# Performance work log

Hardware: AMD Instinct MI355X
Metric: run time of the kernel (lower is better)

The kernel has to match this reference:

```python
import math
import jax, jax.numpy as jnp
import numpy as np

N_HEADS = 32
N_KV_HEADS = 8
HEAD_DIM = 64
DIM = 2048
SEQ = 4096
EST_Q = 64          # idx = min(64, seqlen)
VERTICAL_SIZE = 300 # min(prompt_len, max(300, 30))
SLASH_SIZE = 800    # min(prompt_len, max(800, 50))


def apply_rope(t, cos, sin):
    # t: [B,S,H,hd]; pairs are consecutive (reshape(...,-1,2) in torch view_as_complex)
    B, S, H, hd = t.shape
    tr = t.reshape(B, S, H, hd // 2, 2)
    xr, xi = tr[..., 0], tr[..., 1]
    c = cos[None, :, None, :]
    s = sin[None, :, None, :]
    orr = xr * c - xi * s
    oii = xr * s + xi * c
    return jnp.stack([orr, oii], axis=-1).reshape(B, S, H, hd)


def sum_all_diagonal(mat):
    # faithful jax version of torch as_strided trick: sum over anti-shifted diagonals
    # mat: [b,h,n,m] -> [b,h,n+m-1]; sum_diags[j] = sum_i mat[i, i + j - n], j in [1, n+m-1]
    b, h, n, m = mat.shape
    padded = jnp.pad(mat, ((0, 0), (0, 0), (0, 0), (n, n)))
    gidx = jnp.arange(n)[:, None] + jnp.arange(n + m)[None, :]  # [n, n+m]
    diags = jnp.take_along_axis(padded, jnp.broadcast_to(gidx, (b, h, n, n + m)), axis=-1)
    return diags.sum(axis=2)[:, :, 1:]


def setup_inputs() -> dict:
    key = jax.random.key(0)
    ks = jax.random.split(key, 6)
    x = jax.random.normal(ks[0], (1, SEQ, DIM), dtype=jnp.float32)
    # real RoPE tables (theta = 10000)
    inv_freq = 1.0 / (10000.0 ** (np.arange(0, HEAD_DIM, 2, dtype=np.float32) / HEAD_DIM))
    ang = np.outer(np.arange(SEQ, dtype=np.float32), inv_freq)  # [S, hd/2]
    freqs_cos = jnp.asarray(np.cos(ang), dtype=jnp.float32)
    freqs_sin = jnp.asarray(np.sin(ang), dtype=jnp.float32)
    scale = 0.02
    wq = jax.random.normal(ks[1], (DIM, N_HEADS * HEAD_DIM), dtype=jnp.float32) * scale
    wk = jax.random.normal(ks[2], (DIM, N_KV_HEADS * HEAD_DIM), dtype=jnp.float32) * scale
    wv = jax.random.normal(ks[3], (DIM, N_KV_HEADS * HEAD_DIM), dtype=jnp.float32) * scale
    wo = jax.random.normal(ks[4], (N_HEADS * HEAD_DIM, DIM), dtype=jnp.float32) * scale
    return {"x": x, "freqs_cos": freqs_cos, "freqs_sin": freqs_sin,
            "wq": wq, "wk": wk, "wv": wv, "wo": wo}


def reference(x, freqs_cos, freqs_sin, wq, wk, wv, wo):
    B, S, D = x.shape
    H, Hkv, hd = N_HEADS, N_KV_HEADS, HEAD_DIM
    rep = H // Hkv
    scale = 1.0 / math.sqrt(hd)

    # QKV + RoPE (K gets RoPE, V does not), GQA repeat
    q = apply_rope((x @ wq).reshape(B, S, H, hd), freqs_cos, freqs_sin).transpose(0, 2, 1, 3)
    k = apply_rope((x @ wk).reshape(B, S, Hkv, hd), freqs_cos, freqs_sin)
    v = (x @ wv).reshape(B, S, Hkv, hd)
    k = jnp.repeat(k, rep, axis=2).transpose(0, 2, 1, 3)  # [B,H,S,hd]
    v = jnp.repeat(v, rep, axis=2).transpose(0, 2, 1, 3)

    # --- vertical / slash pattern estimation (first idx queries, as in source) ---
    idx = min(EST_Q, S)
    qe = q[:, :, :idx, :]
    est = jnp.einsum('bhqd,bhkd->bhqk', qe, k) * scale  # [B,H,idx,S]
    ar = jnp.arange(idx)
    blk = ar[:, None] >= ar[None, :]
    tail = jnp.where(blk[None, None], est[..., -idx:], -jnp.inf)
    est = jnp.concatenate([est[..., :S - idx], tail], axis=-1)
    probs = jax.nn.softmax(est, axis=-1)

    Vn = min(S, VERTICAL_SIZE)
    Sl = min(S, SLASH_SIZE)
    vertical = probs.sum(axis=2)                  # [B,H,S]
    _, v_idx = jax.lax.top_k(vertical, Vn)        # [B,H,Vn]
    diag = sum_all_diagonal(probs)[..., :S]       # [..., :-idx+1] -> length S
    _, s_idx = jax.lax.top_k(diag, Sl)
    slash = S - 1 - s_idx                         # [B,H,Sl]

    sparse_keys = jnp.sort(jnp.concatenate([v_idx, slash], axis=-1), axis=-1)  # [B,H,K]

    # --- sparse causal attention over selected keys ---
    k_sp = jnp.take_along_axis(k, sparse_keys[..., None], axis=2)  # [B,H,K,hd]
    v_sp = jnp.take_along_axis(v, sparse_keys[..., None], axis=2)
    att = jnp.einsum('bhqd,bhkd->bhqk', q, k_sp) * scale           # [B,H,S,K]
    causal = sparse_keys[:, :, None, :] <= jnp.arange(S)[None, None, :, None]
    att = jnp.where(causal, att, -1e30)
    p = jax.nn.softmax(att, axis=-1)
    out = jnp.einsum('bhqk,bhkd->bhqd', p, v_sp)
    out = out.transpose(0, 2, 1, 3).reshape(B, S, H * hd)
    return out @ wo
```

## Files before the change

kernel.cpp:

```cpp
#include <hip/hip_runtime.h>
#include <hip/hip_bf16.h>
#include <math.h>
#include <stdint.h>

#define SEQ   4096
#define DIMM  2048
#define NH    32
#define NKV   8
#define HD    64
#define NSP   1100
#define NSPP  1152

typedef __bf16 bf16x8 __attribute__((ext_vector_type(8)));
typedef float  f32x4  __attribute__((ext_vector_type(4)));

__device__ inline void split8(const float* __restrict__ p, bf16x8& h, bf16x8& l) {
#pragma unroll
    for (int i = 0; i < 8; ++i) {
        float v = p[i];
        __bf16 hv = (__bf16)v;
        h[i] = hv;
        l[i] = (__bf16)(v - (float)hv);
    }
}
__device__ inline f32x4 load4(const void* __restrict__ p, size_t idx, bool f) {
    if (f) return *(const f32x4*)((const float*)p + idx);
    const __bf16* b = (const __bf16*)p + idx;
    f32x4 v;
    v[0] = (float)b[0]; v[1] = (float)b[1]; v[2] = (float)b[2]; v[3] = (float)b[3];
    return v;
}
__device__ __forceinline__ void gl_lds16(const __bf16* __restrict__ g, __bf16* l) {
    __builtin_amdgcn_global_load_lds(
        (const __attribute__((address_space(1))) void*)g,
        (__attribute__((address_space(3))) void*)l, 16, 0, 0);
}

__global__ __launch_bounds__(256) void detect_k(const void* __restrict__ x,
                                                int* __restrict__ flag) {
    const __bf16* p = (const __bf16*)x;
    int tid = threadIdx.x;
    bool bad = false;
    for (int i = 0; i < 16; ++i) {
        float v = fabsf((float)p[tid * 16 + i]);
        if (!(v <= 1e10f)) bad = true;
    }
    unsigned long long m = __ballot(bad);
    __shared__ unsigned long long w[4];
    if ((tid & 63) == 0) w[tid >> 6] = m;
    __syncthreads();
    if (tid == 0) flag[0] = ((w[0] | w[1] | w[2] | w[3]) != 0ULL) ? 1 : 0;
}

__global__ __launch_bounds__(256) void convert_x_k(const void* __restrict__ x,
                                                   __bf16* __restrict__ xb,
                                                   const int* __restrict__ flag) {
    int i0 = (blockIdx.x * 256 + threadIdx.x) * 8;
    if (*flag) {
        const float* xf = (const float*)x;
        bf16x8 o;
        for (int i = 0; i < 8; ++i) o[i] = (__bf16)xf[i0 + i];
        *(bf16x8*)(xb + i0) = o;
    } else {
        *(bf16x8*)(xb + i0) = *(const bf16x8*)((const __bf16*)x + i0);
    }
}

__global__ __launch_bounds__(256) void transpose_cvt_k(const void* __restrict__ in,
                                                       __bf16* __restrict__ out, int R, int C,
                                                       const int* __restrict__ flag) {
    __shared__ __bf16 tile[32][33];
    bool f = (*flag != 0);
    int cb = blockIdx.x * 32, rb = blockIdx.y * 32;
    int tx = threadIdx.x & 31, ty = threadIdx.x >> 5;
    for (int i = 0; i < 32; i += 8) {
        size_t idx = (size_t)(rb + ty + i) * C + cb + tx;
        float v = f ? ((const float*)in)[idx] : (float)((const __bf16*)in)[idx];
        tile[ty + i][tx] = (__bf16)v;
    }
    __syncthreads();
    for (int i = 0; i < 32; i += 8)
        out[(size_t)(cb + ty + i) * R + rb + tx] = tile[tx][ty + i];
}

__global__ __launch_bounds__(256) void gemm_nt_k(const __bf16* __restrict__ A,
                                                 const __bf16* __restrict__ Bt,
                                                 void* __restrict__ C, int M, int N, int K,
                                                 int f32out, const int* __restrict__ flag) {
    int bm = blockIdx.x, bn = blockIdx.y;
    __shared__ __bf16 As[128 * 64];
    __shared__ __bf16 Bs[128 * 64];
    int tid = threadIdx.x, wave = tid >> 6, lane = tid & 63;
    int quad = lane >> 4, l16 = lane & 15;
    int wm = (wave >> 1) * 64, wn = (wave & 1) * 64;
    const f32x4 z4 = {0.f, 0.f, 0.f, 0.f};
    f32x4 acc[4][4];
    for (int a = 0; a < 4; ++a) for (int b = 0; b < 4; ++b) acc[a][b] = z4;
    const __bf16* Ab = A  + (size_t)(bm * 128) * K;
    const __bf16* Bb = Bt + (size_t)(bn * 128) * K;
    for (int k0 = 0; k0 < K; k0 += 64) {
#pragma unroll
        for (int it = 0; it < 4; ++it) {
            int ci = it * 256 + tid;
            int row = ci >> 3, c8 = (ci & 7) * 8;
            gl_lds16(Ab + (size_t)row * K + k0 + c8, As + ci * 8);
            gl_lds16(Bb + (size_t)row * K + k0 + c8, Bs + ci * 8);
        }
        __syncthreads();
#pragma unroll
        for (int ks = 0; ks < 2; ++ks) {
            bf16x8 af[4], bfr[4];
#pragma unroll
            for (int mt = 0; mt < 4; ++mt)
                af[mt]  = *(const bf16x8*)&As[(wm + mt * 16 + l16) * 64 + ks * 32 + quad * 8];
#pragma unroll
            for (int nt = 0; nt < 4; ++nt)
                bfr[nt] = *(const bf16x8*)&Bs[(wn + nt * 16 + l16) * 64 + ks * 32 + quad * 8];
#pragma unroll
            for (int mt = 0; mt < 4; ++mt)
#pragma unroll
                for (int nt = 0; nt < 4; ++nt)
                    acc[mt][nt] = __builtin_amdgcn_mfma_f32_16x16x32_bf16(af[mt], bfr[nt], acc[mt][nt], 0, 0, 0);
        }
        __syncthreads();
    }
    bool f32o = f32out && (*flag != 0);
    for (int mt = 0; mt < 4; ++mt)
        for (int nt = 0; nt < 4; ++nt) {
            int rowb = bm * 128 + wm + mt * 16 + quad * 4;
            int col  = bn * 128 + wn + nt * 16 + l16;
            if (f32o) {
                for (int r = 0; r < 4; ++r)
                    ((float*)C)[(size_t)(rowb + r) * N + col] = acc[mt][nt][r];
            } else {
                for (int r = 0; r < 4; ++r)
                    ((__bf16*)C)[(size_t)(rowb + r) * N + col] = (__bf16)acc[mt][nt][r];
            }
        }
}

__device__ __forceinline__ void gemm_split_body(const void* __restrict__ A,
                                                const void* __restrict__ B,
                                                float* __restrict__ C,
                                                int N, int K, bool f, int bm, int bn,
                                                float Asf[][36], float Bsf[][36]) {
    int tid = threadIdx.x, wave = tid >> 6, lane = tid & 63;
    int quad = lane >> 4, l16 = lane & 15;
    int wm = (wave >> 1) * 64, wn = (wave & 1) * 64;
    const f32x4 z4 = {0.f, 0.f, 0.f, 0.f};
    f32x4 acc[4][4];
    for (int a = 0; a < 4; ++a) for (int b = 0; b < 4; ++b) acc[a][b] = z4;
    int arow = tid >> 1, acol = (tid & 1) * 16;
    for (int k0 = 0; k0 < K; k0 += 32) {
        for (int g = 0; g < 4; ++g) {
            f32x4 v = load4(A, (size_t)(bm * 128 + arow) * K + k0 + acol + g * 4, f);
            *(f32x4*)&Asf[arow][acol + g * 4] = v;
        }
        for (int it = 0; it < 4; ++it) {
            int g = tid + it * 256;
            int krow = g >> 5, ng = (g & 31) * 4;
            f32x4 v = load4(B, (size_t)(k0 + krow) * N + bn * 128 + ng, f);
            Bsf[ng + 0][krow] = v[0];
            Bsf[ng + 1][krow] = v[1];
            Bsf[ng + 2][krow] = v[2];
            Bsf[ng + 3][krow] = v[3];
        }
        __syncthreads();
        bf16x8 ah[4], al[4], bh[4], bl[4];
        for (int mt = 0; mt < 4; ++mt) split8(&Asf[wm + mt * 16 + l16][quad * 8], ah[mt], al[mt]);
        for (int nt = 0; nt < 4; ++nt) split8(&Bsf[wn + nt * 16 + l16][quad * 8], bh[nt], bl[nt]);
        for (int mt = 0; mt < 4; ++mt)
            for (int nt = 0; nt < 4; ++nt) {
                acc[mt][nt] = __builtin_amdgcn_mfma_f32_16x16x32_bf16(al[mt], bh[nt], acc[mt][nt], 0, 0, 0);
                acc[mt][nt] = __builtin_amdgcn_mfma_f32_16x16x32_bf16(ah[mt], bl[nt], acc[mt][nt], 0, 0, 0);
                acc[mt][nt] = __builtin_amdgcn_mfma_f32_16x16x32_bf16(ah[mt], bh[nt], acc[mt][nt], 0, 0, 0);
            }
        __syncthreads();
    }
    for (int mt = 0; mt < 4; ++mt)
        for (int nt = 0; nt < 4; ++nt)
            for (int r = 0; r < 4; ++r)
                C[(size_t)(bm * 128 + wm + mt * 16 + quad * 4 + r) * N + bn * 128 + wn + nt * 16 + l16] = acc[mt][nt][r];
}

__global__ __launch_bounds__(256) void gemm_split_dual_k(const void* __restrict__ x,
                                                         const void* __restrict__ wk,
                                                         float* __restrict__ Kf,
                                                         const void* __restrict__ wq,
                                                         float* __restrict__ Qe,
                                                         const int* __restrict__ flag) {
    __shared__ float Asf[128][36];
    __shared__ float Bsf[128][36];
    bool f = (*flag != 0);
    if (blockIdx.x < 32) {
        if (blockIdx.y >= 4) return;
        gemm_split_body(x, wk, Kf, 512, 2048, f, blockIdx.x, blockIdx.y, Asf, Bsf);
    } else {
        gemm_split_body(x, wq, Qe, 2048, 2048, f, 0, blockIdx.y, Asf, Bsf);
    }
}

__global__ __launch_bounds__(256) void rope_all_k(__bf16* __restrict__ Qb,
                                                  float* __restrict__ Kf,
                                                  float* __restrict__ Qe,
                                                  __bf16* __restrict__ Kb,
                                                  const void* __restrict__ fc,
                                                  const void* __restrict__ fs,
                                                  const int* __restrict__ flag) {
    int bx = blockIdx.x;
    bool fl = (*flag != 0);
    if (bx < 4096) {
        int idx = bx * 256 + threadIdx.x;
        int t = idx >> 8;
        int r = idx & 255;
        int hh = r >> 3;
        int j4 = r & 7;
        __bf16* p = Qb + (size_t)t * DIMM + hh * HD + j4 * 8;
        float c[4], s[4];
        if (fl) {
            f32x4 cv = *(const f32x4*)((const float*)fc + t * 32 + j4 * 4);
            f32x4 sv = *(const f32x4*)((const float*)fs + t * 32 + j4 * 4);
#pragma unroll
            for (int i = 0; i < 4; ++i) { c[i] = cv[i]; s[i] = sv[i]; }
        } else {
            const __bf16* cb = (const __bf16*)fc + t * 32 + j4 * 4;
            const __bf16* sb = (const __bf16*)fs + t * 32 + j4 * 4;
#pragma unroll
            for (int i = 0; i < 4; ++i) { c[i] = (float)cb[i]; s[i] = (float)sb[i]; }
        }
        bf16x8 v = *(const bf16x8*)p;
        bf16x8 o;
#pragma unroll
        for (int i = 0; i < 4; ++i) {
            float xr = (float)v[2 * i], xi = (float)v[2 * i + 1];
            o[2 * i]     = (__bf16)(xr * c[i] - xi * s[i]);
            o[2 * i + 1] = (__bf16)(xr * s[i] + xi * c[i]);
        }
        *(bf16x8*)p = o;
    } else {
        int idx = (bx - 4096) * 256 + threadIdx.x;
        const int NKP = SEQ * NKV * 32;
        const int NQP = 64 * NH * 32;
        float* p; int t, j;
        bool isK = (idx < NKP);
        size_t koff = 0;
        if (isK) {
            t = idx >> 8; int r = idx & 255; j = r & 31;
            koff = (size_t)t * (NKV * HD) + (r >> 5) * HD + 2 * j;
            p = Kf + koff;
        } else {
            int k = idx - NKP;
            if (k >= NQP) return;
            t = k >> 10; int r = k & 1023; j = r & 31;
            p = Qe + (size_t)t * DIMM + (r >> 5) * HD + 2 * j;
        }
        float c, s;
        if (fl) {
            c = ((const float*)fc)[t * 32 + j];
            s = ((const float*)fs)[t * 32 + j];
        } else {
            c = (float)((const __bf16*)fc)[t * 32 + j];
            s = (float)((const __bf16*)fs)[t * 32 + j];
        }
        float xr = p[0], xi = p[1];
        float o0 = xr * c - xi * s;
        float o1 = xr * s + xi * c;
        p[0] = o0;
        p[1] = o1;
        if (isK) {
            __bf16* kb = Kb + koff;
            kb[0] = (__bf16)o0;
            kb[1] = (__bf16)o1;
        }
    }
}

__global__ __launch_bounds__(256) void est_part_k(const float* __restrict__ Qe,
                                                  const float* __restrict__ Kf,
                                                  float* __restrict__ pm,
                                                  float* __restrict__ ps,
                                                  float* __restrict__ diag) {
    int h = blockIdx.x, sl = blockIdx.y;
    int tid = threadIdx.x, wave = tid >> 6, lane = tid & 63;
    int quad = lane >> 4, l16 = lane & 15;
    for (int i = tid; i < 512; i += 256) diag[h * SEQ + sl * 512 + i] = 0.f;
    __shared__ float Ml[64];
    __shared__ float pA[4][64];
    bf16x8 qh[4][2], ql[4][2];
    for (int mt = 0; mt < 4; ++mt)
        for (int kc = 0; kc < 2; ++kc)
            split8(Qe + (size_t)(mt * 16 + l16) * DIMM + h * HD + kc * 32 + quad * 8,
                   qh[mt][kc], ql[mt][kc]);
    int kvoff = (h >> 2) * HD;
    float pmax[4][4];
    for (int mt = 0; mt < 4; ++mt) for (int r = 0; r < 4; ++r) pmax[mt][r] = -3.0e38f;
    for (int jb = wave; jb < 8; jb += 4)
        for (int c = 0; c < 4; ++c) {
            int j0 = sl * 512 + jb * 64 + c * 16;
            const float* kp = Kf + (size_t)(j0 + l16) * (NKV * HD) + kvoff + quad * 8;
            bf16x8 kh0, kl0, kh1, kl1;
            split8(kp, kh0, kl0);
            split8(kp + 32, kh1, kl1);
            int j = j0 + l16;
            for (int mt = 0; mt < 4; ++mt) {
                f32x4 acc = {0.f, 0.f, 0.f, 0.f};
                acc = __builtin_amdgcn_mfma_f32_16x16x32_bf16(ql[mt][0], kh0, acc, 0, 0, 0);
                acc = __builtin_amdgcn_mfma_f32_16x16x32_bf16(qh[mt][0], kl0, acc, 0, 0, 0);
                acc = __builtin_amdgcn_mfma_f32_16x16x32_bf16(qh[mt][0], kh0, acc, 0, 0, 0);
                acc = __builtin_amdgcn_mfma_f32_16x16x32_bf16(ql[mt][1], kh1, acc, 0, 0, 0);
                acc = __builtin_amdgcn_mfma_f32_16x16x32_bf16(qh[mt][1], kl1, acc, 0, 0, 0);
                acc = __builtin_amdgcn_mfma_f32_16x16x32_bf16(qh[mt][1], kh1, acc, 0, 0, 0);
                for (int r = 0; r < 4; ++r) {
                    int q = mt * 16 + quad * 4 + r;
                    float sv = acc[r] * 0.125f;
                    if (j >= SEQ - 64 && q < j - (SEQ - 64)) sv = -1e30f;
                    pmax[mt][r] = fmaxf(pmax[mt][r], sv);
                }
            }
        }
    for (int mt = 0; mt < 4; ++mt)
        for (int r = 0; r < 4; ++r)
            for (int m2 = 1; m2 < 16; m2 <<= 1)
                pmax[mt][r] = fmaxf(pmax[mt][r], __shfl_xor(pmax[mt][r], m2));
    if (l16 == 0)
        for (int mt = 0; mt < 4; ++mt)
            for (int r = 0; r < 4; ++r)
                pA[wave][mt * 16 + quad * 4 + r] = pmax[mt][r];
    __syncthreads();
    if (tid < 64)
        Ml[tid] = fmaxf(fmaxf(pA[0][tid], pA[1][tid]), fmaxf(pA[2][tid], pA[3][tid]));
    __syncthreads();
    float mreg[4][4];
    for (int mt = 0; mt < 4; ++mt)
        for (int r = 0; r < 4; ++r)
            mreg[mt][r] = Ml[mt * 16 + quad * 4 + r];
    float psum[4][4];
    for (int mt = 0; mt < 4; ++mt) for (int r = 0; r < 4; ++r) psum[mt][r] = 0.f;
    for (int jb = wave; jb < 8; jb += 4)
        for (int c = 0; c < 4; ++c) {
            int j0 = sl * 512 + jb * 64 + c * 16;
            const float* kp = Kf + (size_t)(j0 + l16) * (NKV * HD) + kvoff + quad * 8;
            bf16x8 kh0, kl0, kh1, kl1;
            split8(kp, kh0, kl0);
            split8(kp + 32, kh1, kl1);
            int j = j0 + l16;
            for (int mt = 0; mt < 4; ++mt) {
                f32x4 acc = {0.f, 0.f, 0.f, 0.f};
                acc = __builtin_amdgcn_mfma_f32_16x16x32_bf16(ql[mt][0], kh0, acc, 0, 0, 0);
                acc = __builtin_amdgcn_mfma_f32_16x16x32_bf16(qh[mt][0], kl0, acc, 0, 0, 0);
                acc = __builtin_amdgcn_mfma_f32_16x16x32_bf16(qh[mt][0], kh0, acc, 0, 0, 0);
                acc = __builtin_amdgcn_mfma_f32_16x16x32_bf16(ql[mt][1], kh1, acc, 0, 0, 0);
                acc = __builtin_amdgcn_mfma_f32_16x16x32_bf16(qh[mt][1], kl1, acc, 0, 0, 0);
                acc = __builtin_amdgcn_mfma_f32_16x16x32_bf16(qh[mt][1], kh1, acc, 0, 0, 0);
                for (int r = 0; r < 4; ++r) {
                    int q = mt * 16 + quad * 4 + r;
                    float sv = acc[r] * 0.125f;
                    if (j >= SEQ - 64 && q < j - (SEQ - 64)) sv = -1e30f;
                    psum[mt][r] += __expf(sv - mreg[mt][r]);
                }
            }
        }
    for (int mt = 0; mt < 4; ++mt)
        for (int r = 0; r < 4; ++r)
            for (int m2 = 1; m2 < 16; m2 <<= 1)
                psum[mt][r] += __shfl_xor(psum[mt][r], m2);
    if (l16 == 0)
        for (int mt = 0; mt < 4; ++mt)
            for (int r = 0; r < 4; ++r)
                pA[wave][mt * 16 + quad * 4 + r] = psum[mt][r];
    __syncthreads();
    if (tid < 64) {
        pm[(h * 8 + sl) * 64 + tid] = Ml[tid];
        ps[(h * 8 + sl) * 64 + tid] = pA[0][tid] + pA[1][tid] + pA[2][tid] + pA[3][tid];
    }
}

__global__ __launch_bounds__(256) void vert_diag_k(const float* __restrict__ Qe,
                                                   const float* __restrict__ Kf,
                                                   const float* __restrict__ pm,
                                                   const float* __restrict__ ps,
                                                   float* __restrict__ vert,
                                                   float* __restrict__ diag) {
    int h = blockIdx.x, jb = blockIdx.y;
    int tid = threadIdx.x, wave = tid >> 6, lane = tid & 63;
    int quad = lane >> 4, l16 = lane & 15;
    __shared__ float P[64][132];
    __shared__ float dloc[192];
    __shared__ float rm_l[64], rs_l[64];
    for (int i = tid; i < 192; i += 256) dloc[i] = 0.f;
    if (tid < 64) {
        float M = -3.0e38f;
        for (int sl = 0; sl < 8; ++sl) M = fmaxf(M, pm[(h * 8 + sl) * 64 + tid]);
        float S = 0.f;
        for (int sl = 0; sl < 8; ++sl)
            S += ps[(h * 8 + sl) * 64 + tid] * __expf(pm[(h * 8 + sl) * 64 + tid] - M);
        rm_l[tid] = M;
        rs_l[tid] = S;
    }
    bf16x8 qh[4][2], ql[4][2];
    for (int mt = 0; mt < 4; ++mt)
        for (int kc = 0; kc < 2; ++kc)
            split8(Qe + (size_t)(mt * 16 + l16) * DIMM + h * HD + kc * 32 + quad * 8,
                   qh[mt][kc], ql[mt][kc]);
    __syncthreads();
    float rm[4][4], rs[4][4];
    for (int mt = 0; mt < 4; ++mt)
        for (int r = 0; r < 4; ++r) {
            int q = mt * 16 + quad * 4 + r;
            rm[mt][r] = rm_l[q];
            rs[mt][r] = rs_l[q];
        }
    int kvoff = (h >> 2) * HD;
    for (int c = 0; c < 2; ++c) {
        int jl0 = wave * 32 + c * 16;
        int j0 = jb * 128 + jl0;
        const float* kp = Kf + (size_t)(j0 + l16) * (NKV * HD) + kvoff + quad * 8;
        bf16x8 kh0, kl0, kh1, kl1;
        split8(kp, kh0, kl0);
        split8(kp + 32, kh1, kl1);
        int j = j0 + l16;
        for (int mt = 0; mt < 4; ++mt) {
            f32x4 acc = {0.f, 0.f, 0.f, 0.f};
            acc = __builtin_amdgcn_mfma_f32_16x16x32_bf16(ql[mt][0], kh0, acc, 0, 0, 0);
            acc = __builtin_amdgcn_mfma_f32_16x16x32_bf16(qh[mt][0], kl0, acc, 0, 0, 0);
            acc = __builtin_amdgcn_mfma_f32_16x16x32_bf16(qh[mt][0], kh0, acc, 0, 0, 0);
            acc = __builtin_amdgcn_mfma_f32_16x16x32_bf16(ql[mt][1], kh1, acc, 0, 0, 0);
            acc = __builtin_amdgcn_mfma_f32_16x16x32_bf16(qh[mt][1], kl1, acc, 0, 0, 0);
            acc = __builtin_amdgcn_mfma_f32_16x16x32_bf16(qh[mt][1], kh1, acc, 0, 0, 0);
            for (int r = 0; r < 4; ++r) {
                int q = mt * 16 + quad * 4 + r;
                float sv = acc[r] * 0.125f;
                if (j >= SEQ - 64 && q < j - (SEQ - 64)) sv = -1e30f;
                P[q][jl0 + l16] = __expf(sv - rm[mt][r]) / rs[mt][r];
            }
        }
    }
    __syncthreads();
    if (tid < 128) {
        float vacc = 0.f;
        for (int q = 0; q < 64; ++q) {
            float pb = P[q][tid];
            vacc += pb;
            if (jb * 128 + tid + 63 - q < SEQ) atomicAdd(&dloc[tid + 63 - q], pb);
        }
        vert[h * SEQ + jb * 128 + tid] = vacc;
    }
    __syncthreads();
    for (int i = tid; i < 192; i += 256) {
        int g = jb * 128 + i;
        if (g < SEQ) atomicAdd(&diag[h * SEQ + g], dloc[i]);
    }
}

__global__ __launch_bounds__(256) void topk_merge_k(const float* __restrict__ vert,
                                                    const float* __restrict__ diag,
                                                    int* __restrict__ skeys) {
    __shared__ int cnt[4096];
    __shared__ int hist4[4][256];
    __shared__ int scanb[256];
    __shared__ int B_sh, kk_sh;
    int h = blockIdx.x, tid = threadIdx.x, wave = tid >> 6;
    for (int i = tid; i < 4096; i += 256) cnt[i] = 0;
    __syncthreads();
    for (int selp = 0; selp < 2; ++selp) {
        const float* vals = (selp == 0 ? vert : diag) + h * SEQ;
        int k = (selp == 0) ? 300 : 800;
        bool flip = (selp == 1);
        unsigned bits[16];
        for (int g = 0; g < 4; ++g) {
            f32x4 v = *(const f32x4*)(vals + tid * 16 + g * 4);
            for (int e = 0; e < 4; ++e) bits[g * 4 + e] = __float_as_uint(v[e]);
        }
        unsigned prefix = 0;
        int kk = k;
        for (int pass = 0; pass < 4; ++pass) {
            int sh = 8 * (3 - pass);
            for (int w = 0; w < 4; ++w) hist4[w][tid] = 0;
            __syncthreads();
            for (int e = 0; e < 16; ++e) {
                unsigned b = bits[e];
                bool in = (pass == 0) || ((b >> (sh + 8)) == prefix);
                if (in) atomicAdd(&hist4[wave][(b >> sh) & 255], 1);
            }
            __syncthreads();
            scanb[tid] = hist4[0][tid] + hist4[1][tid] + hist4[2][tid] + hist4[3][tid];
            __syncthreads();
            for (int off = 1; off < 256; off <<= 1) {
                int v = (tid + off < 256) ? scanb[tid + off] : 0;
                __syncthreads();
                scanb[tid] += v;
                __syncthreads();
            }
            int sufNext = (tid < 255) ? scanb[tid + 1] : 0;
            if (scanb[tid] >= kk && sufNext < kk) { B_sh = tid; kk_sh = kk - sufNext; }
            __syncthreads();
            prefix = (prefix << 8) | (unsigned)B_sh;
            kk = kk_sh;
            __syncthreads();
        }
        int localEq = 0;
        for (int e = 0; e < 16; ++e) {
            unsigned b = bits[e];
            if (b > prefix) {
                int idx = tid * 16 + e;
                atomicAdd(&cnt[flip ? (4095 - idx) : idx], 1);
            } else if (b == prefix) ++localEq;
        }
        scanb[tid] = localEq;
        __syncthreads();
        for (int off = 1; off < 256; off <<= 1) {
            int v = (tid >= off) ? scanb[tid - off] : 0;
            __syncthreads();
            scanb[tid] += v;
            __syncthreads();
        }
        int eqOff = scanb[tid] - localEq;
        int taken = 0;
        for (int e = 0; e < 16; ++e) {
            unsigned b = bits[e];
            if (b == prefix) {
                if (eqOff + taken < kk) {
                    int idx = tid * 16 + e;
                    atomicAdd(&cnt[flip ? (4095 - idx) : idx], 1);
                }
                ++taken;
            }
        }
        __syncthreads();
    }
    int base = tid * 16;
    int loc[16];
    int s = 0;
    for (int e = 0; e < 16; ++e) { loc[e] = s; s += cnt[base + e]; }
    scanb[tid] = s;
    __syncthreads();
    for (int off = 1; off < 256; off <<= 1) {
        int v = (tid >= off) ? scanb[tid - off] : 0;
        __syncthreads();
        scanb[tid] += v;
        __syncthreads();
    }
    int chunkExcl = scanb[tid] - s;
    int* out = skeys + h * NSPP;
    for (int e = 0; e < 16; ++e) {
        int c = cnt[base + e];
        int pos = chunkExcl + loc[e];
        for (int r = 0; r < c; ++r) out[pos + r] = base + e;
    }
    for (int i = NSP + tid; i < NSPP; i += 256) out[i] = 0x7fffffff;
}

__global__ __launch_bounds__(256) void gather_k(const __bf16* __restrict__ Kb,
                                                const __bf16* __restrict__ Vb,
                                                const int* __restrict__ skeys,
                                                __bf16* __restrict__ Ksp,
                                                __bf16* __restrict__ VspT) {
    int h = blockIdx.x, jb = blockIdx.y;
    __shared__ __bf16 tile[64][72];
    int tid = threadIdx.x;
    int jl = tid >> 2, d0 = (tid & 3) * 16;
    int j = jb * 64 + jl;
    int key = skeys[h * NSPP + j];
    int kv = (h >> 2) * HD;
    const bf16x8 z = {};
    bf16x8 k0v = z, k1v = z, v0v = z, v1v = z;
    if ((unsigned)key < SEQ) {
        const __bf16* ks = Kb + (size_t)key * (NKV * HD) + kv + d0;
        const __bf16* vs = Vb + (size_t)key * (NKV * HD) + kv + d0;
        k0v = *(const bf16x8*)ks; k1v = *(const bf16x8*)(ks + 8);
        v0v = *(const bf16x8*)vs; v1v = *(const bf16x8*)(vs + 8);
    }
    __bf16* kd = Ksp + ((size_t)h * NSPP + j) * HD + d0;
    *(bf16x8*)kd = k0v;
    *(bf16x8*)(kd + 8) = k1v;
    *(bf16x8*)&tile[jl][d0] = v0v;
    *(bf16x8*)&tile[jl][d0 + 8] = v1v;
    __syncthreads();
    int d = tid >> 2, jl0 = (tid & 3) * 16;
    bf16x8 o0, o1;
    for (int e = 0; e < 8; ++e) { o0[e] = tile[jl0 + e][d]; o1[e] = tile[jl0 + 8 + e][d]; }
    __bf16* vt = VspT + ((size_t)h * HD + d) * NSPP + jb * 64 + jl0;
    *(bf16x8*)vt = o0;
    *(bf16x8*)(vt + 8) = o1;
}

__global__ __launch_bounds__(512) void sparse_attn_k(const __bf16* __restrict__ Qb,
                                                     const __bf16* __restrict__ Ksp,
                                                     const __bf16* __restrict__ VspT,
                                                     const int* __restrict__ skeys,
                                                     __bf16* __restrict__ AO) {
    int qb = blockIdx.x, h = blockIdx.y;
    int tid = threadIdx.x, wave = tid >> 6, lane = tid & 63;
    int quad = lane >> 4, l16 = lane & 15;
    __shared__ __bf16 sc[64][1160];
    __shared__ float rsm[64];
    int t0 = qb * 64;
    bf16x8 aq[4][2];
#pragma unroll
    for (int qs = 0; qs < 4; ++qs)
#pragma unroll
        for (int kc = 0; kc < 2; ++kc)
            aq[qs][kc] = *(const bf16x8*)(Qb + (size_t)(t0 + qs * 16 + l16) * DIMM + h * HD + kc * 32 + quad * 8);
    const __bf16* Kh = Ksp + (size_t)h * NSPP * HD;
    const int* sk = skeys + h * NSPP;
#pragma unroll
    for (int c = 0; c < 9; ++c) {
        int j0 = wave * 144 + c * 16;
        const __bf16* kp = Kh + (size_t)(j0 + l16) * HD + quad * 8;
        bf16x8 b0 = *(const bf16x8*)kp;
        bf16x8 b1 = *(const bf16x8*)(kp + 32);
        int j = j0 + l16;
        int key = sk[j];
#pragma unroll
        for (int qs = 0; qs < 4; ++qs) {
            f32x4 acc = {0.f, 0.f, 0.f, 0.f};
            acc = __builtin_amdgcn_mfma_f32_16x16x32_bf16(aq[qs][0], b0, acc, 0, 0, 0);
            acc = __builtin_amdgcn_mfma_f32_16x16x32_bf16(aq[qs][1], b1, acc, 0, 0, 0);
            int qg = t0 + qs * 16 + quad * 4;
#pragma unroll
            for (int r = 0; r < 4; ++r) {
                float sv = acc[r] * 0.125f;
                if (key > qg + r) sv = -1e30f;
                sc[qs * 16 + quad * 4 + r][j] = (__bf16)sv;
            }
        }
    }
    __syncthreads();
    {
        int row = tid >> 3, sub = tid & 7;
        int c0 = sub * 144;
        float mx = -3.0e38f;
        for (int i = 0; i < 18; ++i) {
            bf16x8 v = *(const bf16x8*)&sc[row][c0 + i * 8];
            for (int e = 0; e < 8; ++e) mx = fmaxf(mx, (float)v[e]);
        }
        for (int m2 = 1; m2 < 8; m2 <<= 1) mx = fmaxf(mx, __shfl_xor(mx, m2, 8));
        float sm = 0.f;
        for (int i = 0; i < 18; ++i) {
            int cb = c0 + i * 8;
            bf16x8 v = *(const bf16x8*)&sc[row][cb];
            bf16x8 pw;
            for (int e = 0; e < 8; ++e) {
                float pv = 0.f;
                if (cb + e < NSP) { pv = __expf((float)v[e] - mx); sm += pv; }
                pw[e] = (__bf16)pv;
            }
            *(bf16x8*)&sc[row][cb] = pw;
        }
        for (int m2 = 1; m2 < 8; m2 <<= 1) sm += __shfl_xor(sm, m2, 8);
        if (sub == 0) rsm[row] = sm;
    }
    __syncthreads();
    int qs = wave >> 1, dh = wave & 1;
    const f32x4 z4 = {0.f, 0.f, 0.f, 0.f};
    f32x4 o0 = z4, o1 = z4;
    const __bf16* Vh = VspT + ((size_t)h * HD + dh * 32) * NSPP;
#pragma unroll 4
    for (int c = 0; c < 36; ++c) {
        int kb = c * 32;
        bf16x8 pa = *(const bf16x8*)&sc[qs * 16 + l16][kb + quad * 8];
        bf16x8 v0 = *(const bf16x8*)(Vh + (size_t)l16 * NSPP + kb + quad * 8);
        bf16x8 v1 = *(const bf16x8*)(Vh + (size_t)(16 + l16) * NSPP + kb + quad * 8);
        o0 = __builtin_amdgcn_mfma_f32_16x16x32_bf16(pa, v0, o0, 0, 0, 0);
        o1 = __builtin_amdgcn_mfma_f32_16x16x32_bf16(pa, v1, o1, 0, 0, 0);
    }
#pragma unroll
    for (int r = 0; r < 4; ++r) {
        int ql = qs * 16 + quad * 4 + r;
        float inv = 1.f / rsm[ql];
        size_t base = (size_t)(t0 + ql) * DIMM + h * HD + dh * 32;
        AO[base + l16]      = (__bf16)(o0[r] * inv);
        AO[base + 16 + l16] = (__bf16)(o1[r] * inv);
    }
}

extern "C" void kernel_launch(void* const* d_in, const int* in_sizes, int n_in,
                              void* d_out, int out_size, void* d_ws, size_t ws_size,
                              hipStream_t stream) {
    const void* x  = d_in[0];
    const void* fc = d_in[1];
    const void* fs = d_in[2];
    const void* wq = d_in[3];
    const void* wk = d_in[4];
    const void* wv = d_in[5];
    const void* wo = d_in[6];
    char* ws = (char*)d_ws;

    __bf16* Qb   = (__bf16*)(ws + 0);
    __bf16* Kb   = (__bf16*)(ws + 16777216);
    __bf16* Vb   = (__bf16*)(ws + 20971520);
    __bf16* xbf  = (__bf16*)(ws + 25165824);
    float*  Kf32 = (float*)(ws + 25165824);
    float*  Qef32= (float*)(ws + 33554432);
    __bf16* AO   = (__bf16*)(ws + 25165824);
    __bf16* Wt   = (__bf16*)(ws + 41943040);
    __bf16* Ksp  = (__bf16*)(ws + 41943040);
    __bf16* VspT = (__bf16*)(ws + 46661632);
    float*  vert = (float*)(ws + 51396608);
    float*  diag = (float*)(ws + 51920896);
    int*    skeys= (int*)(ws + 52445184);
    int*    flag = (int*)(ws + 52592640);
    float*  pm   = (float*)(ws + 52592896);
    float*  ps   = (float*)(ws + 52658432);

    dim3 b256(256);
    detect_k<<<1, b256, 0, stream>>>(x, flag);
    convert_x_k<<<4096, b256, 0, stream>>>(x, xbf, flag);
    transpose_cvt_k<<<dim3(64, 64), b256, 0, stream>>>(wq, Wt, 2048, 2048, flag);
    gemm_nt_k<<<dim3(32, 16), b256, 0, stream>>>(xbf, Wt, Qb, 4096, 2048, 2048, 0, flag);
    transpose_cvt_k<<<dim3(16, 64), b256, 0, stream>>>(wv, Wt, 2048, 512, flag);
    gemm_nt_k<<<dim3(32, 4), b256, 0, stream>>>(xbf, Wt, Vb, 4096, 512, 2048, 0, flag);
    gemm_split_dual_k<<<dim3(33, 16), b256, 0, stream>>>(x, wk, Kf32, wq, Qef32, flag);
    rope_all_k<<<8448, b256, 0, stream>>>(Qb, Kf32, Qef32, Kb, fc, fs, flag);
    est_part_k<<<dim3(32, 8), b256, 0, stream>>>(Qef32, Kf32, pm, ps, diag);
    vert_diag_k<<<dim3(32, 32), b256, 0, stream>>>(Qef32, Kf32, pm, ps, vert, diag);
    topk_merge_k<<<32, b256, 0, stream>>>(vert, diag, skeys);
    gather_k<<<dim3(32, 18), b256, 0, stream>>>(Kb, Vb, skeys, Ksp, VspT);
    sparse_attn_k<<<dim3(64, 32), dim3(512), 0, stream>>>(Qb, Ksp, VspT, skeys, AO);
    transpose_cvt_k<<<dim3(64, 64), b256, 0, stream>>>(wo, Wt, 2048, 2048, flag);
    gemm_nt_k<<<dim3(32, 16), b256, 0, stream>>>(AO, Wt, d_out, 4096, 2048, 2048, 1, flag);
}
```

Baseline: 871.2 us.

## Fuse projections and RoPE into one launch, drop weight transposes

Replaces the separate weight transpose/convert kernels with an NN GEMM that reads the row-major weights directly, converts them to bf16 and writes them transposed into LDS. Q, V, K and the estimation-Q projections are merged into a single launch, with RoPE applied in the GEMM epilogue through a lane-pair shuffle, which removes the standalone rope kernel. The goal is to cut launches and the extra global round trips for transposed weights and RoPE. In exchange, B-tile loads become strided scalar LDS stores on the critical path, and the combined grid mixes different block kinds with uneven work.

```diff
diff --git a/kernel.cpp b/kernel.cpp
--- a/kernel.cpp
+++ b/kernel.cpp
@@ -14,6 +14,10 @@
 typedef __bf16 bf16x8 __attribute__((ext_vector_type(8)));
 typedef float  f32x4  __attribute__((ext_vector_type(4)));
 
+#define MODE_V 0
+#define MODE_Q 1
+#define MODE_O 2
+
 __device__ inline void split8(const float* __restrict__ p, bf16x8& h, bf16x8& l) {
 #pragma unroll
     for (int i = 0; i < 8; ++i) {
@@ -34,6 +38,16 @@
     __builtin_amdgcn_global_load_lds(
         (const __attribute__((address_space(1))) void*)g,
         (__attribute__((address_space(3))) void*)l, 16, 0, 0);
+}
+__device__ __forceinline__ void cs_at(const void* fc, const void* fs, bool f,
+                                      int t, int j, float& c, float& s) {
+    if (f) {
+        c = ((const float*)fc)[t * 32 + j];
+        s = ((const float*)fs)[t * 32 + j];
+    } else {
+        c = (float)((const __bf16*)fc)[t * 32 + j];
+        s = (float)((const __bf16*)fs)[t * 32 + j];
+    }
 }
 
 __global__ __launch_bounds__(256) void detect_k(const void* __restrict__ x,
@@ -66,45 +80,39 @@
     }
 }
 
-__global__ __launch_bounds__(256) void transpose_cvt_k(const void* __restrict__ in,
-                                                       __bf16* __restrict__ out, int R, int C,
-                                                       const int* __restrict__ flag) {
-    __shared__ __bf16 tile[32][33];
-    bool f = (*flag != 0);
-    int cb = blockIdx.x * 32, rb = blockIdx.y * 32;
-    int tx = threadIdx.x & 31, ty = threadIdx.x >> 5;
-    for (int i = 0; i < 32; i += 8) {
-        size_t idx = (size_t)(rb + ty + i) * C + cb + tx;
-        float v = f ? ((const float*)in)[idx] : (float)((const __bf16*)in)[idx];
-        tile[ty + i][tx] = (__bf16)v;
-    }
-    __syncthreads();
-    for (int i = 0; i < 32; i += 8)
-        out[(size_t)(cb + ty + i) * R + rb + tx] = tile[tx][ty + i];
-}
-
-__global__ __launch_bounds__(256) void gemm_nt_k(const __bf16* __restrict__ A,
-                                                 const __bf16* __restrict__ Bt,
-                                                 void* __restrict__ C, int M, int N, int K,
-                                                 int f32out, const int* __restrict__ flag) {
-    int bm = blockIdx.x, bn = blockIdx.y;
-    __shared__ __bf16 As[128 * 64];
-    __shared__ __bf16 Bs[128 * 64];
+__device__ __forceinline__ void gemm_nn_body(const __bf16* __restrict__ A,
+                                             const void* __restrict__ B,
+                                             void* __restrict__ C, int N,
+                                             int bm, int bn, bool f, int mode,
+                                             const void* __restrict__ fc,
+                                             const void* __restrict__ fs,
+                                             char* smem) {
+    const int K = DIMM;
+    __bf16* As = (__bf16*)smem;
+    __bf16 (*Bs)[72] = (__bf16 (*)[72])(smem + 16384);
     int tid = threadIdx.x, wave = tid >> 6, lane = tid & 63;
     int quad = lane >> 4, l16 = lane & 15;
     int wm = (wave >> 1) * 64, wn = (wave & 1) * 64;
     const f32x4 z4 = {0.f, 0.f, 0.f, 0.f};
     f32x4 acc[4][4];
     for (int a = 0; a < 4; ++a) for (int b = 0; b < 4; ++b) acc[a][b] = z4;
-    const __bf16* Ab = A  + (size_t)(bm * 128) * K;
-    const __bf16* Bb = Bt + (size_t)(bn * 128) * K;
+    const __bf16* Ab = A + (size_t)(bm * 128) * K;
     for (int k0 = 0; k0 < K; k0 += 64) {
 #pragma unroll
         for (int it = 0; it < 4; ++it) {
             int ci = it * 256 + tid;
             int row = ci >> 3, c8 = (ci & 7) * 8;
             gl_lds16(Ab + (size_t)row * K + k0 + c8, As + ci * 8);
-            gl_lds16(Bb + (size_t)row * K + k0 + c8, Bs + ci * 8);
+        }
+#pragma unroll
+        for (int it = 0; it < 8; ++it) {
+            int g = tid + it * 256;
+            int krow = g >> 5, ng = (g & 31) * 4;
+            f32x4 v = load4(B, (size_t)(k0 + krow) * N + bn * 128 + ng, f);
+            Bs[ng + 0][krow] = (__bf16)v[0];
+            Bs[ng + 1][krow] = (__bf16)v[1];
+            Bs[ng + 2][krow] = (__bf16)v[2];
+            Bs[ng + 3][krow] = (__bf16)v[3];
         }
         __syncthreads();
 #pragma unroll
@@ -112,10 +120,10 @@
             bf16x8 af[4], bfr[4];
 #pragma unroll
             for (int mt = 0; mt < 4; ++mt)
-                af[mt]  = *(const bf16x8*)&As[(wm + mt * 16 + l16) * 64 + ks * 32 + quad * 8];
+                af[mt] = *(const bf16x8*)&As[(wm + mt * 16 + l16) * 64 + ks * 32 + quad * 8];
 #pragma unroll
             for (int nt = 0; nt < 4; ++nt)
-                bfr[nt] = *(const bf16x8*)&Bs[(wn + nt * 16 + l16) * 64 + ks * 32 + quad * 8];
+                bfr[nt] = *(const bf16x8*)&Bs[wn + nt * 16 + l16][ks * 32 + quad * 8];
 #pragma unroll
             for (int mt = 0; mt < 4; ++mt)
 #pragma unroll
@@ -124,26 +132,58 @@
         }
         __syncthreads();
     }
-    bool f32o = f32out && (*flag != 0);
-    for (int mt = 0; mt < 4; ++mt)
-        for (int nt = 0; nt < 4; ++nt) {
-            int rowb = bm * 128 + wm + mt * 16 + quad * 4;
-            int col  = bn * 128 + wn + nt * 16 + l16;
-            if (f32o) {
-                for (int r = 0; r < 4; ++r)
-                    ((float*)C)[(size_t)(rowb + r) * N + col] = acc[mt][nt][r];
-            } else {
+    if (mode == MODE_Q) {
+        for (int mt = 0; mt < 4; ++mt)
+            for (int nt = 0; nt < 4; ++nt)
+#pragma unroll
+                for (int r = 0; r < 4; ++r) {
+                    int col = bn * 128 + wn + nt * 16 + l16;
+                    int t = bm * 128 + wm + mt * 16 + quad * 4 + r;
+                    float qv = (float)(__bf16)acc[mt][nt][r];
+                    float pv = __shfl_xor(qv, 1);
+                    int j = (col & 63) >> 1;
+                    float c, s;
+                    cs_at(fc, fs, f, t, j, c, s);
+                    float o = (lane & 1) ? (pv * s + qv * c) : (qv * c - pv * s);
+                    ((__bf16*)C)[(size_t)t * N + col] = (__bf16)o;
+                }
+    } else if (mode == MODE_O) {
+        bool f32o = f;
+        for (int mt = 0; mt < 4; ++mt)
+            for (int nt = 0; nt < 4; ++nt) {
+                int rowb = bm * 128 + wm + mt * 16 + quad * 4;
+                int col = bn * 128 + wn + nt * 16 + l16;
+                if (f32o) {
+                    for (int r = 0; r < 4; ++r)
+                        ((float*)C)[(size_t)(rowb + r) * N + col] = acc[mt][nt][r];
+                } else {
+                    for (int r = 0; r < 4; ++r)
+                        ((__bf16*)C)[(size_t)(rowb + r) * N + col] = (__bf16)acc[mt][nt][r];
+                }
+            }
+    } else {
+        for (int mt = 0; mt < 4; ++mt)
+            for (int nt = 0; nt < 4; ++nt) {
+                int rowb = bm * 128 + wm + mt * 16 + quad * 4;
+                int col = bn * 128 + wn + nt * 16 + l16;
                 for (int r = 0; r < 4; ++r)
                     ((__bf16*)C)[(size_t)(rowb + r) * N + col] = (__bf16)acc[mt][nt][r];
             }
-        }
-}
-
-__device__ __forceinline__ void gemm_split_body(const void* __restrict__ A,
-                                                const void* __restrict__ B,
-                                                float* __restrict__ C,
-                                                int N, int K, bool f, int bm, int bn,
-                                                float Asf[][36], float Bsf[][36]) {
+    }
+}
+
+__device__ __forceinline__ void gemm_split_rope_body(const void* __restrict__ A,
+                                                     const void* __restrict__ B,
+                                                     float* __restrict__ C,
+                                                     __bf16* __restrict__ Cb,
+                                                     int N, bool f, int bm, int bn,
+                                                     bool ropeAll,
+                                                     const void* __restrict__ fc,
+                                                     const void* __restrict__ fs,
+                                                     char* smem) {
+    const int K = DIMM;
+    float (*Asf)[36] = (float (*)[36])smem;
+    float (*Bsf)[36] = (float (*)[36])(smem + 18432);
     int tid = threadIdx.x, wave = tid >> 6, lane = tid & 63;
     int quad = lane >> 4, l16 = lane & 15;
     int wm = (wave >> 1) * 64, wn = (wave & 1) * 64;
@@ -179,100 +219,60 @@
     }
     for (int mt = 0; mt < 4; ++mt)
         for (int nt = 0; nt < 4; ++nt)
-            for (int r = 0; r < 4; ++r)
-                C[(size_t)(bm * 128 + wm + mt * 16 + quad * 4 + r) * N + bn * 128 + wn + nt * 16 + l16] = acc[mt][nt][r];
-}
-
-__global__ __launch_bounds__(256) void gemm_split_dual_k(const void* __restrict__ x,
-                                                         const void* __restrict__ wk,
-                                                         float* __restrict__ Kf,
-                                                         const void* __restrict__ wq,
-                                                         float* __restrict__ Qe,
-                                                         const int* __restrict__ flag) {
-    __shared__ float Asf[128][36];
-    __shared__ float Bsf[128][36];
-    bool f = (*flag != 0);
-    if (blockIdx.x < 32) {
-        if (blockIdx.y >= 4) return;
-        gemm_split_body(x, wk, Kf, 512, 2048, f, blockIdx.x, blockIdx.y, Asf, Bsf);
-    } else {
-        gemm_split_body(x, wq, Qe, 2048, 2048, f, 0, blockIdx.y, Asf, Bsf);
-    }
-}
-
-__global__ __launch_bounds__(256) void rope_all_k(__bf16* __restrict__ Qb,
+#pragma unroll
+            for (int r = 0; r < 4; ++r) {
+                int col = bn * 128 + wn + nt * 16 + l16;
+                int t = bm * 128 + wm + mt * 16 + quad * 4 + r;
+                float v = acc[mt][nt][r];
+                float pv = __shfl_xor(v, 1);
+                float o = v;
+                if (ropeAll || t < 64) {
+                    int j = (col & 63) >> 1;
+                    float c, s;
+                    cs_at(fc, fs, f, t, j, c, s);
+                    o = (lane & 1) ? (pv * s + v * c) : (v * c - pv * s);
+                }
+                C[(size_t)t * N + col] = o;
+                if (ropeAll) Cb[(size_t)t * N + col] = (__bf16)o;
+            }
+}
+
+__global__ __launch_bounds__(256) void proj_all_k(const __bf16* __restrict__ xbf,
+                                                  const void* __restrict__ x,
+                                                  const void* __restrict__ wq,
+                                                  const void* __restrict__ wv,
+                                                  const void* __restrict__ wk,
+                                                  __bf16* __restrict__ Qb,
+                                                  __bf16* __restrict__ Vb,
                                                   float* __restrict__ Kf,
                                                   float* __restrict__ Qe,
                                                   __bf16* __restrict__ Kb,
                                                   const void* __restrict__ fc,
                                                   const void* __restrict__ fs,
                                                   const int* __restrict__ flag) {
-    int bx = blockIdx.x;
-    bool fl = (*flag != 0);
-    if (bx < 4096) {
-        int idx = bx * 256 + threadIdx.x;
-        int t = idx >> 8;
-        int r = idx & 255;
-        int hh = r >> 3;
-        int j4 = r & 7;
-        __bf16* p = Qb + (size_t)t * DIMM + hh * HD + j4 * 8;
-        float c[4], s[4];
-        if (fl) {
-            f32x4 cv = *(const f32x4*)((const float*)fc + t * 32 + j4 * 4);
-            f32x4 sv = *(const f32x4*)((const float*)fs + t * 32 + j4 * 4);
-#pragma unroll
-            for (int i = 0; i < 4; ++i) { c[i] = cv[i]; s[i] = sv[i]; }
-        } else {
-            const __bf16* cb = (const __bf16*)fc + t * 32 + j4 * 4;
-            const __bf16* sb = (const __bf16*)fs + t * 32 + j4 * 4;
-#pragma unroll
-            for (int i = 0; i < 4; ++i) { c[i] = (float)cb[i]; s[i] = (float)sb[i]; }
-        }
-        bf16x8 v = *(const bf16x8*)p;
-        bf16x8 o;
-#pragma unroll
-        for (int i = 0; i < 4; ++i) {
-            float xr = (float)v[2 * i], xi = (float)v[2 * i + 1];
-            o[2 * i]     = (__bf16)(xr * c[i] - xi * s[i]);
-            o[2 * i + 1] = (__bf16)(xr * s[i] + xi * c[i]);
-        }
-        *(bf16x8*)p = o;
+    __shared__ __align__(16) char smem[36864];
+    bool f = (*flag != 0);
+    int bx = blockIdx.x, by = blockIdx.y;
+    if (bx < 32) {
+        gemm_nn_body(xbf, wq, Qb, 2048, bx, by, f, MODE_Q, fc, fs, smem);
+    } else if (bx < 40) {
+        int bm = (bx - 32) * 4 + (by >> 2), bn = by & 3;
+        gemm_nn_body(xbf, wv, Vb, 512, bm, bn, f, MODE_V, fc, fs, smem);
+    } else if (bx < 48) {
+        int bm = (bx - 40) * 4 + (by >> 2), bn = by & 3;
+        gemm_split_rope_body(x, wk, Kf, Kb, 512, f, bm, bn, true, fc, fs, smem);
     } else {
-        int idx = (bx - 4096) * 256 + threadIdx.x;
-        const int NKP = SEQ * NKV * 32;
-        const int NQP = 64 * NH * 32;
-        float* p; int t, j;
-        bool isK = (idx < NKP);
-        size_t koff = 0;
-        if (isK) {
-            t = idx >> 8; int r = idx & 255; j = r & 31;
-            koff = (size_t)t * (NKV * HD) + (r >> 5) * HD + 2 * j;
-            p = Kf + koff;
-        } else {
-            int k = idx - NKP;
-            if (k >= NQP) return;
-            t = k >> 10; int r = k & 1023; j = r & 31;
-            p = Qe + (size_t)t * DIMM + (r >> 5) * HD + 2 * j;
-        }
-        float c, s;
-        if (fl) {
-            c = ((const float*)fc)[t * 32 + j];
-            s = ((const float*)fs)[t * 32 + j];
-        } else {
-            c = (float)((const __bf16*)fc)[t * 32 + j];
-            s = (float)((const __bf16*)fs)[t * 32 + j];
-        }
-        float xr = p[0], xi = p[1];
-        float o0 = xr * c - xi * s;
-        float o1 = xr * s + xi * c;
-        p[0] = o0;
-        p[1] = o1;
-        if (isK) {
-            __bf16* kb = Kb + koff;
-            kb[0] = (__bf16)o0;
-            kb[1] = (__bf16)o1;
-        }
-    }
+        gemm_split_rope_body(x, wq, Qe, nullptr, 2048, f, 0, by, false, fc, fs, smem);
+    }
+}
+
+__global__ __launch_bounds__(256) void gemm_nn_o_k(const __bf16* __restrict__ A,
+                                                   const void* __restrict__ B,
+                                                   void* __restrict__ C,
+                                                   const int* __restrict__ flag) {
+    __shared__ __align__(16) char smem[36864];
+    bool f = (*flag != 0);
+    gemm_nn_body(A, B, C, 2048, blockIdx.x, blockIdx.y, f, MODE_O, nullptr, nullptr, smem);
 }
 
 __global__ __launch_bounds__(256) void est_part_k(const float* __restrict__ Qe,
@@ -690,10 +690,9 @@
     __bf16* Kb   = (__bf16*)(ws + 16777216);
     __bf16* Vb   = (__bf16*)(ws + 20971520);
     __bf16* xbf  = (__bf16*)(ws + 25165824);
-    float*  Kf32 = (float*)(ws + 25165824);
-    float*  Qef32= (float*)(ws + 33554432);
     __bf16* AO   = (__bf16*)(ws + 25165824);
-    __bf16* Wt   = (__bf16*)(ws + 41943040);
+    float*  Kf32 = (float*)(ws + 41943040);
+    float*  Qef32= (float*)(ws + 50331648);
     __bf16* Ksp  = (__bf16*)(ws + 41943040);
     __bf16* VspT = (__bf16*)(ws + 46661632);
     float*  vert = (float*)(ws + 51396608);
@@ -706,17 +705,13 @@
     dim3 b256(256);
     detect_k<<<1, b256, 0, stream>>>(x, flag);
     convert_x_k<<<4096, b256, 0, stream>>>(x, xbf, flag);
-    transpose_cvt_k<<<dim3(64, 64), b256, 0, stream>>>(wq, Wt, 2048, 2048, flag);
-    gemm_nt_k<<<dim3(32, 16), b256, 0, stream>>>(xbf, Wt, Qb, 4096, 2048, 2048, 0, flag);
-    transpose_cvt_k<<<dim3(16, 64), b256, 0, stream>>>(wv, Wt, 2048, 512, flag);
-    gemm_nt_k<<<dim3(32, 4), b256, 0, stream>>>(xbf, Wt, Vb, 4096, 512, 2048, 0, flag);
-    gemm_split_dual_k<<<dim3(33, 16), b256, 0, stream>>>(x, wk, Kf32, wq, Qef32, flag);
-    rope_all_k<<<8448, b256, 0, stream>>>(Qb, Kf32, Qef32, Kb, fc, fs, flag);
+    proj_all_k<<<dim3(49, 16), b256, 0, stream>>>(xbf, x, wq, wv, wk,
+                                                  Qb, Vb, Kf32, Qef32, Kb,
+                                                  fc, fs, flag);
     est_part_k<<<dim3(32, 8), b256, 0, stream>>>(Qef32, Kf32, pm, ps, diag);
     vert_diag_k<<<dim3(32, 32), b256, 0, stream>>>(Qef32, Kf32, pm, ps, vert, diag);
     topk_merge_k<<<32, b256, 0, stream>>>(vert, diag, skeys);
     gather_k<<<dim3(32, 18), b256, 0, stream>>>(Kb, Vb, skeys, Ksp, VspT);
     sparse_attn_k<<<dim3(64, 32), dim3(512), 0, stream>>>(Qb, Ksp, VspT, skeys, AO);
-    transpose_cvt_k<<<dim3(64, 64), b256, 0, stream>>>(wo, Wt, 2048, 2048, flag);
-    gemm_nt_k<<<dim3(32, 16), b256, 0, stream>>>(AO, Wt, d_out, 4096, 2048, 2048, 1, flag);
-}
+    gemm_nn_o_k<<<dim3(32, 16), b256, 0, stream>>>(AO, wo, d_out, flag);
+}
```

Measured after the change: 1.044 ms. 1.2x slower.
